# Performance work log

Measured on AMD Instinct MI355X. Metric: run time of the kernel, lower is better.

## Reference

```python
import jax, jax.numpy as jnp
import numpy as np

N_HID = 256
N_IN = 2
N_OUT = 2
BATCH = 256
LENGTH = 1024
ALPHA = 0.25
SIGMA_NEU = 0.05
N_CON = 6553


def setup_inputs() -> dict:
    key = jax.random.key(0)
    k1, k2, k3, k4, k5 = jax.random.split(key, 5)
    rng = np.random.RandomState(0)
    # masked recurrent weight pieces (match torch __init__ construction)
    w_0 = rng.randn(N_HID, N_HID) / np.sqrt(N_HID)
    abs_w_0 = jnp.asarray(np.abs(w_0), dtype=jnp.float32)
    is_con_np = np.zeros((N_HID, N_HID), dtype=np.float32)
    ind_in = rng.choice(np.arange(N_HID), size=N_CON)
    ind_out = rng.choice(np.arange(N_HID), size=N_CON)
    is_con_np[ind_in, ind_out] = 1.0
    w_sign = jnp.asarray(np.sign(rng.randn(N_HID, N_HID)), dtype=jnp.float32)
    is_con = jnp.asarray(is_con_np)
    return {
        "input_signal": jax.random.normal(k1, (BATCH, LENGTH, N_IN), dtype=jnp.float32),
        "hidden": jnp.zeros((BATCH, N_HID), dtype=jnp.float32),
        "w_in": jax.random.normal(k2, (N_HID, N_IN), dtype=jnp.float32) / np.sqrt(N_IN),
        "w_out": jax.random.normal(k3, (N_OUT, N_HID), dtype=jnp.float32) / np.sqrt(N_HID),
        "abs_w_0": abs_w_0,
        "w_sign": w_sign,
        "is_con": is_con,
    }


def reference(input_signal, hidden, w_in, w_out, abs_w_0, w_sign, is_con):
    # masked signed recurrent weight: theta = |w0| * mask; w_hh = sign * theta where mask>0
    theta = abs_w_0 * is_con
    w_hh = jnp.where(is_con > 0, w_sign * theta, jnp.zeros_like(theta))  # [H,H]

    alpha = jnp.full((N_HID,), ALPHA, dtype=input_signal.dtype)
    x = jnp.transpose(input_signal, (1, 0, 2))  # [T,B,I]
    # input projection for all timesteps at once (w_in has no bias)
    inp_proj = jnp.einsum("tbi,hi->tbh", x, w_in)  # [T,B,H]
    # iid per-step neural noise: randn * sigma * sqrt(alpha)
    noise = (jax.random.normal(jax.random.key(42), (LENGTH, BATCH, N_HID), dtype=input_signal.dtype)
             * SIGMA_NEU * jnp.sqrt(alpha))

    def step(h, uv):
        u, n = uv
        tmp = u + jnp.tanh(h) @ w_hh.T  # F.linear(tanh(h), w_hh)
        h_new = (1.0 - alpha) * h + alpha * tmp + n
        return h_new, h_new

    h_last, hs = jax.lax.scan(step, hidden, (inp_proj, noise))  # hs: [T,B,H]
    outputs = jnp.einsum("tbh,oh->tbo", hs, w_out)  # [T,B,O]
    hidden_list = jnp.transpose(hs, (1, 0, 2))  # [B,T,H]
    output_list = jnp.transpose(outputs, (1, 0, 2))  # [B,T,O]
    return hidden_list, output_list, h_last
```

## Files before the change

kernel.cpp:

```cpp
#include <hip/hip_runtime.h>
#include <stdint.h>

#define TT 1024
#define HB 256
#define NE 48
#define O1 67108864u
#define O2 (67108864u + 524288u)

__device__ __forceinline__ uint32_t rotl32(uint32_t x, uint32_t r){ return (x<<r)|(x>>(32u-r)); }

#define RND(r) { x0+=x1; x1=rotl32(x1,(r)); x1^=x0; }
__device__ __forceinline__ void tf_h1g(uint32_t k0,uint32_t k1,uint32_t ks2,uint32_t& x0,uint32_t& x1){
  x0 += k0; x1 += k1;
  RND(13) RND(15) RND(26) RND(6)  x0+=k1;  x1+=ks2+1u;
  RND(17) RND(29) RND(16) RND(24) x0+=ks2; x1+=k0+2u;
  RND(13) RND(15) RND(26) RND(6)  x0+=k0;  x1+=k1+3u;
}
__device__ __forceinline__ void tf_h2g(uint32_t k0,uint32_t k1,uint32_t ks2,uint32_t& x0,uint32_t& x1){
  RND(17) RND(29) RND(16) RND(24) x0+=k1;  x1+=ks2+4u;
  RND(13) RND(15) RND(26) RND(6)  x0+=ks2; x1+=k0+5u;
}
__device__ __forceinline__ void tf2x32(uint32_t k0,uint32_t k1,uint32_t& x0,uint32_t& x1){
  const uint32_t ks2 = 0x1BD11BDAu ^ k0 ^ k1;
  tf_h1g(k0,k1,ks2,x0,x1); tf_h2g(k0,k1,ks2,x0,x1);
}
__device__ __forceinline__ void tf_h1(uint32_t& x0, uint32_t& x1){ tf_h1g(0u,42u,0x1BD11BF0u,x0,x1); }
__device__ __forceinline__ void tf_h2(uint32_t& x0, uint32_t& x1){ tf_h2g(0u,42u,0x1BD11BF0u,x0,x1); }
#undef RND

__device__ __forceinline__ float bits_to_noise(uint32_t bits){
  float f = __uint_as_float((bits>>9) | 0x3F800000u) - 1.0f;
  const float lo = -0.99999994f;
  float x = fmaxf(fmaf(f, 1.99999994f, lo), lo);
  float m = (1.0f - x) * (1.0f + x);
  float w = -0.69314718056f * __log2f(m);
  float p;
  if (w < 5.0f){
    w -= 2.5f;
    p = 2.81022636e-08f;
    p = fmaf(p, w, 3.43273939e-07f);
    p = fmaf(p, w, -3.5233877e-06f);
    p = fmaf(p, w, -4.39150654e-06f);
    p = fmaf(p, w, 0.00021858087f);
    p = fmaf(p, w, -0.00125372503f);
    p = fmaf(p, w, -0.00417768164f);
    p = fmaf(p, w, 0.246640727f);
    p = fmaf(p, w, 1.50140941f);
  } else {
    w = __fsqrt_rn(w) - 3.0f;
    p = -0.000200214257f;
    p = fmaf(p, w, 0.000100950558f);
    p = fmaf(p, w, 0.00134934322f);
    p = fmaf(p, w, -0.00367342844f);
    p = fmaf(p, w, 0.00573950773f);
    p = fmaf(p, w, -0.0076224613f);
    p = fmaf(p, w, 0.00943887047f);
    p = fmaf(p, w, 1.00167406f);
    p = fmaf(p, w, 2.83297682f);
  }
  return 0.035355339059f * (p * x);
}

__global__ void init_flags(uint32_t* flags){
  if (flags) { flags[0]=0u; flags[1]=0u; }
}

__global__ void check_kernel(float* out, const uint32_t* flags){
  uint32_t a0=0u, a1=0u;                 tf2x32(0u,0u,a0,a1);
  uint32_t b0=0xffffffffu, b1=0xffffffffu; tf2x32(0xffffffffu,0xffffffffu,b0,b1);
  uint32_t c0=0x243f6a88u, c1=0x85a308d3u; tf2x32(0x13198a2eu,0x03707344u,c0,c1);
  if (!(a0==0x6b200159u && a1==0x99ba4efeu)) out[0] = 1e30f;
  if (!(b0==0x1cb996fcu && b1==0xbb002be7u)) out[1] = 2e30f;
  if (!(c0==0xc4923a9cu && c1==0x483df7a0u)) out[2] = 3e30f;
  uint32_t d0=7u, d1=9u; tf_h1(d0,d1); tf_h2(d0,d1);
  uint32_t e0=7u, e1=9u; tf2x32(0u,42u,e0,e1);
  if (!(d0==e0 && d1==e1)) out[3] = 4e30f;
  if (flags && flags[0]) out[5] = 6e30f;
}

__launch_bounds__(512)
__global__ void rnn_kernel(const float* __restrict__ input_signal,
                           const float* __restrict__ hidden0,
                           const float* __restrict__ w_in,
                           const float* __restrict__ w_out,
                           const float* __restrict__ abs_w0,
                           const float* __restrict__ w_sign,
                           const float* __restrict__ is_con,
                           float* __restrict__ out,
                           uint32_t* __restrict__ flags)
{
  __shared__ float    ew[HB][NE];
  __shared__ uint16_t ei[HB][NE];
  __shared__ float    xbuf[TT*2];
  __shared__ float    hstage[8][HB];
  __shared__ float    nbuf[4][HB];
  __shared__ float    tbuf[2][HB];
  __shared__ int      cnts[HB];
  __shared__ int      rankinv[HB];
  __shared__ int      rof4[HB];
  __shared__ float    wot0[HB], wot1[HB];

  const int tid = threadIdx.x;
  const int b   = blockIdx.x;
  const bool gw = (tid < HB);

  {
    const float* xg = input_signal + (uint64_t)b*TT*2;
    *(float4*)(xbuf + tid*4) = *(const float4*)(xg + tid*4);
  }
  if (gw){
    int c = 0;
    const float* ic = is_con + tid*HB;
    for (int k = 0; k < HB; k += 4){
      float4 c4 = *(const float4*)(ic + k);
      c += (c4.x>0.f)+(c4.y>0.f)+(c4.z>0.f)+(c4.w>0.f);
    }
    cnts[tid] = c;
    if (c > NE && flags) flags[0] = 1u;
  }
  __syncthreads();

  if (gw){
    int myc = cnts[tid], r = 0;
    for (int k = 0; k < HB; ++k){
      int ck = cnts[k];
      r += (int)((ck > myc) || (ck == myc && k < tid));
    }
    rankinv[r] = tid;
    rof4[tid]  = r << 2;
  }
  __syncthreads();

  uint32_t bj = 0u, ax0 = 0u, ax1 = 0u;
  if (gw){
    const int j = tid;
    const float* ic = is_con + j*HB;
    const float* aw = abs_w0 + j*HB;
    const float* ws = w_sign + j*HB;
    int n = 0;
    for (int k = 0; k < HB; ++k){
      if (ic[k] > 0.f && n < NE){
        ew[j][n] = ws[k]*aw[k];
        ei[j][n] = (uint16_t)rof4[k];
        ++n;
      }
    }
    for (int s = n; s < NE; ++s){ ew[j][s] = 0.f; ei[j][s] = (uint16_t)rof4[j]; }
    wot0[rof4[j]>>2] = w_out[j];
    wot1[rof4[j]>>2] = w_out[HB + j];
  } else {
    int m = tid - HB;
    int rowm = rankinv[m];
    bj = (uint32_t)b*256u + (uint32_t)rowm;
    uint32_t x0 = 0u, x1 = bj;
    tf2x32(0u, 42u, x0, x1);
    nbuf[0][m] = bits_to_noise(x0 ^ x1);
    ax0 = 0u; ax1 = 65536u + bj;
    tf_h1(ax0, ax1);
  }
  __syncthreads();

  float    pwv[NE];
  uint32_t piv[NE/2];
  int trip = 0, row = 0;
  float h = 0.f, wi0 = 0.f, wi1 = 0.f;
  float4 wo0 = {0,0,0,0}, wo1 = {0,0,0,0};
  if (gw){
    row = rankinv[tid];
    #pragma unroll
    for (int s = 0; s < NE; ++s) pwv[s] = ew[row][s];
    #pragma unroll
    for (int s = 0; s < NE/2; ++s) piv[s] = *(const uint32_t*)(&ei[row][2*s]);
    int c = cnts[row];
    trip = __builtin_amdgcn_readfirstlane((c + 3) & ~3);
    h   = hidden0[b*HB + row];
    wi0 = w_in[row*2]; wi1 = w_in[row*2 + 1];
    tbuf[0][tid] = 1.0f - 2.0f/(__expf(2.0f*h) + 1.0f);
  } else if (tid < HB + 64){
    int lam = tid - HB;
    wo0 = *(const float4*)(wot0 + lam*4);
    wo1 = *(const float4*)(wot1 + lam*4);
  }
  float* hrow = out + (uint64_t)b*TT*HB;
  float* orow = out + O1 + (uint64_t)b*TT*2;
  __syncthreads();

  for (int t = 0; t < TT; ++t){
    const int par = t & 1;
    if (gw){
      const char* tb = (const char*)(&tbuf[par][0]);
      float y0 = 0.f, y1 = 0.f;
      #pragma unroll
      for (int s = 0; s < NE; s += 4){
        if (s < trip){
          uint32_t pa = piv[s>>1], pb = piv[(s>>1)+1];
          float t0 = *(const float*)(tb + (pa & 0xFFFFu));
          float t1 = *(const float*)(tb + (pa >> 16));
          float t2 = *(const float*)(tb + (pb & 0xFFFFu));
          float t3 = *(const float*)(tb + (pb >> 16));
          y0 = fmaf(pwv[s+0], t0, y0);
          y1 = fmaf(pwv[s+1], t1, y1);
          y0 = fmaf(pwv[s+2], t2, y0);
          y1 = fmaf(pwv[s+3], t3, y1);
        }
      }
      float nz = nbuf[t&3][tid];
      float2 xv = *(const float2*)(xbuf + t*2);
      float u  = fmaf(xv.x, wi0, xv.y*wi1);
      h = fmaf(0.25f, u + y0 + y1, 0.75f*h) + nz;
      hstage[t&7][tid] = h;
      tbuf[par^1][tid] = 1.0f - 2.0f/(__expf(2.0f*h) + 1.0f);
    } else {
      int m = tid - HB;
      if (t < TT-1){
        uint32_t f0 = ax0, f1 = ax1;
        tf_h2(f0, f1);
        nbuf[(t+1)&3][m] = bits_to_noise(f0 ^ f1);
      }
      if (t < TT-2){
        ax0 = 0u; ax1 = (uint32_t)(t+2)*65536u + bj;
        tf_h1(ax0, ax1);
      }
      if (m < 64 && t > 0){
        float4 hv = *(const float4*)(&hstage[(t-1)&7][m*4]);
        float p0 = hv.x*wo0.x + hv.y*wo0.y + hv.z*wo0.z + hv.w*wo0.w;
        float p1 = hv.x*wo1.x + hv.y*wo1.y + hv.z*wo1.z + hv.w*wo1.w;
        #pragma unroll
        for (int d = 1; d < 64; d <<= 1){
          p0 += __shfl_xor(p0, d, 64);
          p1 += __shfl_xor(p1, d, 64);
        }
        if (m == 0) *(float2*)(orow + (t-1)*2) = make_float2(p0, p1);
      }
    }
    __syncthreads();

    if ((t & 7) == 7){
      int s  = tid >> 6;
      int j0 = (tid & 63) << 2;
      int4 rk = *(const int4*)(rof4 + j0);
      const char* hs = (const char*)(&hstage[s][0]);
      float4 v;
      v.x = *(const float*)(hs + rk.x);
      v.y = *(const float*)(hs + rk.y);
      v.z = *(const float*)(hs + rk.z);
      v.w = *(const float*)(hs + rk.w);
      *(float4*)(hrow + (uint64_t)(t - 7 + s)*HB + j0) = v;
      __syncthreads();
    }
  }

  if (!gw && (tid - HB) < 64){
    int m = tid - HB;
    float4 hv = *(const float4*)(&hstage[7][m*4]);
    float p0 = hv.x*wo0.x + hv.y*wo0.y + hv.z*wo0.z + hv.w*wo0.w;
    float p1 = hv.x*wo1.x + hv.y*wo1.y + hv.z*wo1.z + hv.w*wo1.w;
    #pragma unroll
    for (int d = 1; d < 64; d <<= 1){
      p0 += __shfl_xor(p0, d, 64);
      p1 += __shfl_xor(p1, d, 64);
    }
    if (m == 0) *(float2*)(orow + (TT-1)*2) = make_float2(p0, p1);
  }
  if (gw) out[O2 + b*HB + row] = h;
}

extern "C" void kernel_launch(void* const* d_in, const int* in_sizes, int n_in,
                              void* d_out, int out_size, void* d_ws, size_t ws_size,
                              hipStream_t stream) {
  const float* input_signal = (const float*)d_in[0];
  const float* hidden       = (const float*)d_in[1];
  const float* w_in         = (const float*)d_in[2];
  const float* w_out        = (const float*)d_in[3];
  const float* abs_w0       = (const float*)d_in[4];
  const float* w_sign       = (const float*)d_in[5];
  const float* is_con       = (const float*)d_in[6];
  float* out = (float*)d_out;
  uint32_t* flags = (ws_size >= 8) ? (uint32_t*)d_ws : nullptr;

  init_flags<<<1, 1, 0, stream>>>(flags);
  rnn_kernel<<<256, 512, 0, stream>>>(input_signal, hidden, w_in, w_out,
                                      abs_w0, w_sign, is_con, out, flags);
  check_kernel<<<1, 1, 0, stream>>>(out, flags);
}
```

Baseline: 1.023 ms.

## Split each hidden row across two lanes and double block size to 1024 threads

The block grows from 512 to 1024 threads. Each recurrent row is now computed by two lanes, each handling half of the sparse entries, and the halves are combined with a shuffle, which halves the serial per-step gather chain. The noise-generation and output-projection threads are also reorganised: 512 helper threads alternate between computing two timesteps of noise on even steps and projecting two delayed hidden states on odd steps. In exchange there are more waves per barrier, a shuffle on the critical path, idle odd lanes during the update, and the per-row register budget is halved under the larger launch bound.

```diff
diff --git a/kernel.cpp b/kernel.cpp
--- a/kernel.cpp
+++ b/kernel.cpp
@@ -4,28 +4,22 @@
 #define TT 1024
 #define HB 256
 #define NE 48
+#define NE2 24
 #define O1 67108864u
 #define O2 (67108864u + 524288u)
 
 __device__ __forceinline__ uint32_t rotl32(uint32_t x, uint32_t r){ return (x<<r)|(x>>(32u-r)); }
 
 #define RND(r) { x0+=x1; x1=rotl32(x1,(r)); x1^=x0; }
-__device__ __forceinline__ void tf_h1g(uint32_t k0,uint32_t k1,uint32_t ks2,uint32_t& x0,uint32_t& x1){
+__device__ __forceinline__ void tf2x32(uint32_t k0,uint32_t k1,uint32_t& x0,uint32_t& x1){
+  const uint32_t ks2 = 0x1BD11BDAu ^ k0 ^ k1;
   x0 += k0; x1 += k1;
   RND(13) RND(15) RND(26) RND(6)  x0+=k1;  x1+=ks2+1u;
   RND(17) RND(29) RND(16) RND(24) x0+=ks2; x1+=k0+2u;
   RND(13) RND(15) RND(26) RND(6)  x0+=k0;  x1+=k1+3u;
-}
-__device__ __forceinline__ void tf_h2g(uint32_t k0,uint32_t k1,uint32_t ks2,uint32_t& x0,uint32_t& x1){
   RND(17) RND(29) RND(16) RND(24) x0+=k1;  x1+=ks2+4u;
   RND(13) RND(15) RND(26) RND(6)  x0+=ks2; x1+=k0+5u;
 }
-__device__ __forceinline__ void tf2x32(uint32_t k0,uint32_t k1,uint32_t& x0,uint32_t& x1){
-  const uint32_t ks2 = 0x1BD11BDAu ^ k0 ^ k1;
-  tf_h1g(k0,k1,ks2,x0,x1); tf_h2g(k0,k1,ks2,x0,x1);
-}
-__device__ __forceinline__ void tf_h1(uint32_t& x0, uint32_t& x1){ tf_h1g(0u,42u,0x1BD11BF0u,x0,x1); }
-__device__ __forceinline__ void tf_h2(uint32_t& x0, uint32_t& x1){ tf_h2g(0u,42u,0x1BD11BF0u,x0,x1); }
 #undef RND
 
 __device__ __forceinline__ float bits_to_noise(uint32_t bits){
@@ -72,13 +66,10 @@
   if (!(a0==0x6b200159u && a1==0x99ba4efeu)) out[0] = 1e30f;
   if (!(b0==0x1cb996fcu && b1==0xbb002be7u)) out[1] = 2e30f;
   if (!(c0==0xc4923a9cu && c1==0x483df7a0u)) out[2] = 3e30f;
-  uint32_t d0=7u, d1=9u; tf_h1(d0,d1); tf_h2(d0,d1);
-  uint32_t e0=7u, e1=9u; tf2x32(0u,42u,e0,e1);
-  if (!(d0==e0 && d1==e1)) out[3] = 4e30f;
   if (flags && flags[0]) out[5] = 6e30f;
 }
 
-__launch_bounds__(512)
+__launch_bounds__(1024)
 __global__ void rnn_kernel(const float* __restrict__ input_signal,
                            const float* __restrict__ hidden0,
                            const float* __restrict__ w_in,
@@ -102,13 +93,13 @@
 
   const int tid = threadIdx.x;
   const int b   = blockIdx.x;
-  const bool gw = (tid < HB);
+  const bool gw = (tid < 512);
 
   {
     const float* xg = input_signal + (uint64_t)b*TT*2;
-    *(float4*)(xbuf + tid*4) = *(const float4*)(xg + tid*4);
-  }
-  if (gw){
+    *(float2*)(xbuf + tid*2) = *(const float2*)(xg + tid*2);
+  }
+  if (tid < HB){
     int c = 0;
     const float* ic = is_con + tid*HB;
     for (int k = 0; k < HB; k += 4){
@@ -120,7 +111,7 @@
   }
   __syncthreads();
 
-  if (gw){
+  if (tid < HB){
     int myc = cnts[tid], r = 0;
     for (int k = 0; k < HB; ++k){
       int ck = cnts[k];
@@ -131,8 +122,8 @@
   }
   __syncthreads();
 
-  uint32_t bj = 0u, ax0 = 0u, ax1 = 0u;
-  if (gw){
+  uint32_t bj = 0u;
+  if (tid < HB){
     const int j = tid;
     const float* ic = is_con + j*HB;
     const float* aw = abs_w0 + j*HB;
@@ -148,38 +139,54 @@
     for (int s = n; s < NE; ++s){ ew[j][s] = 0.f; ei[j][s] = (uint16_t)rof4[j]; }
     wot0[rof4[j]>>2] = w_out[j];
     wot1[rof4[j]>>2] = w_out[HB + j];
-  } else {
-    int m = tid - HB;
-    int rowm = rankinv[m];
-    bj = (uint32_t)b*256u + (uint32_t)rowm;
-    uint32_t x0 = 0u, x1 = bj;
-    tf2x32(0u, 42u, x0, x1);
-    nbuf[0][m] = bits_to_noise(x0 ^ x1);
-    ax0 = 0u; ax1 = 65536u + bj;
-    tf_h1(ax0, ax1);
-  }
-  __syncthreads();
-
-  float    pwv[NE];
-  uint32_t piv[NE/2];
-  int trip = 0, row = 0;
+  } else if (tid >= 512){
+    int m = tid - 512, rn = m >> 1, qn = m & 1;
+    bj = (uint32_t)b*256u + (uint32_t)rankinv[rn];
+    if (qn == 0){
+      uint32_t x0 = 0u, x1 = bj;
+      tf2x32(0u, 42u, x0, x1);
+      nbuf[0][rn] = bits_to_noise(x0 ^ x1);
+    }
+  }
+  __syncthreads();
+
+  float    pwv[NE2];
+  uint32_t piv[NE2/2];
+  int trip = 0, row = 0, q = 0, rr = 0;
   float h = 0.f, wi0 = 0.f, wi1 = 0.f;
   float4 wo0 = {0,0,0,0}, wo1 = {0,0,0,0};
+  int rf0 = 0, rf1 = 0;
+  {
+    int j0 = (tid & 127) << 1;
+    rf0 = rof4[j0]; rf1 = rof4[j0+1];
+  }
   if (gw){
-    row = rankinv[tid];
+    rr = tid >> 1; q = tid & 1;
+    row = rankinv[rr];
+    int c = cnts[row]; if (c > NE) c = NE;
+    uint16_t pad = (uint16_t)rof4[row];
+    uint32_t cur = 0u;
     #pragma unroll
-    for (int s = 0; s < NE; ++s) pwv[s] = ew[row][s];
-    #pragma unroll
-    for (int s = 0; s < NE/2; ++s) piv[s] = *(const uint32_t*)(&ei[row][2*s]);
-    int c = cnts[row];
-    trip = __builtin_amdgcn_readfirstlane((c + 3) & ~3);
-    h   = hidden0[b*HB + row];
-    wi0 = w_in[row*2]; wi1 = w_in[row*2 + 1];
-    tbuf[0][tid] = 1.0f - 2.0f/(__expf(2.0f*h) + 1.0f);
-  } else if (tid < HB + 64){
-    int lam = tid - HB;
-    wo0 = *(const float4*)(wot0 + lam*4);
-    wo1 = *(const float4*)(wot1 + lam*4);
+    for (int s = 0; s < NE2; ++s){
+      int idx = 2*s + q;
+      float w = 0.f; uint32_t o = pad;
+      if (idx < c){ w = ew[row][idx]; o = ei[row][idx]; }
+      pwv[s] = w;
+      if (s & 1) piv[s>>1] = cur | (o << 16); else cur = o;
+    }
+    trip = __builtin_amdgcn_readfirstlane((c + 1) >> 1);
+    if (q == 0){
+      h   = hidden0[b*HB + row];
+      wi0 = w_in[row*2]; wi1 = w_in[row*2 + 1];
+      tbuf[0][rr] = 1.0f - 2.0f/(__expf(2.0f*h) + 1.0f);
+    }
+  } else {
+    int m = tid - 512;
+    if (m < 128){
+      int lam = m & 63;
+      wo0 = *(const float4*)(wot0 + lam*4);
+      wo1 = *(const float4*)(wot1 + lam*4);
+    }
   }
   float* hrow = out + (uint64_t)b*TT*HB;
   float* orow = out + O1 + (uint64_t)b*TT*2;
@@ -191,78 +198,79 @@
       const char* tb = (const char*)(&tbuf[par][0]);
       float y0 = 0.f, y1 = 0.f;
       #pragma unroll
-      for (int s = 0; s < NE; s += 4){
+      for (int s = 0; s < NE2; s += 2){
         if (s < trip){
-          uint32_t pa = piv[s>>1], pb = piv[(s>>1)+1];
+          uint32_t pa = piv[s>>1];
           float t0 = *(const float*)(tb + (pa & 0xFFFFu));
           float t1 = *(const float*)(tb + (pa >> 16));
-          float t2 = *(const float*)(tb + (pb & 0xFFFFu));
-          float t3 = *(const float*)(tb + (pb >> 16));
-          y0 = fmaf(pwv[s+0], t0, y0);
+          y0 = fmaf(pwv[s],   t0, y0);
           y1 = fmaf(pwv[s+1], t1, y1);
-          y0 = fmaf(pwv[s+2], t2, y0);
-          y1 = fmaf(pwv[s+3], t3, y1);
         }
       }
-      float nz = nbuf[t&3][tid];
-      float2 xv = *(const float2*)(xbuf + t*2);
-      float u  = fmaf(xv.x, wi0, xv.y*wi1);
-      h = fmaf(0.25f, u + y0 + y1, 0.75f*h) + nz;
-      hstage[t&7][tid] = h;
-      tbuf[par^1][tid] = 1.0f - 2.0f/(__expf(2.0f*h) + 1.0f);
+      float y = y0 + y1;
+      y += __shfl_xor(y, 1, 64);
+      if (q == 0){
+        float nz = nbuf[t&3][rr];
+        float2 xv = *(const float2*)(xbuf + t*2);
+        float u  = fmaf(xv.x, wi0, xv.y*wi1);
+        h = fmaf(0.25f, u + y, 0.75f*h) + nz;
+        hstage[t&7][rr] = h;
+        tbuf[par^1][rr] = 1.0f - 2.0f/(__expf(2.0f*h) + 1.0f);
+      }
     } else {
-      int m = tid - HB;
-      if (t < TT-1){
-        uint32_t f0 = ax0, f1 = ax1;
-        tf_h2(f0, f1);
-        nbuf[(t+1)&3][m] = bits_to_noise(f0 ^ f1);
-      }
-      if (t < TT-2){
-        ax0 = 0u; ax1 = (uint32_t)(t+2)*65536u + bj;
-        tf_h1(ax0, ax1);
-      }
-      if (m < 64 && t > 0){
-        float4 hv = *(const float4*)(&hstage[(t-1)&7][m*4]);
-        float p0 = hv.x*wo0.x + hv.y*wo0.y + hv.z*wo0.z + hv.w*wo0.w;
-        float p1 = hv.x*wo1.x + hv.y*wo1.y + hv.z*wo1.z + hv.w*wo1.w;
-        #pragma unroll
-        for (int d = 1; d < 64; d <<= 1){
-          p0 += __shfl_xor(p0, d, 64);
-          p1 += __shfl_xor(p1, d, 64);
+      int m = tid - 512;
+      if (!(t & 1)){
+        int tv = t + 1 + (m & 1);
+        if (tv < TT){
+          uint32_t x0 = 0u, x1 = (uint32_t)tv*65536u + bj;
+          tf2x32(0u, 42u, x0, x1);
+          nbuf[tv&3][m>>1] = bits_to_noise(x0 ^ x1);
         }
-        if (m == 0) *(float2*)(orow + (t-1)*2) = make_float2(p0, p1);
+      } else if (m < 128){
+        int tau = t - 2 + (m >> 6);
+        if (tau >= 0){
+          int lam = m & 63;
+          float4 hv = *(const float4*)(&hstage[tau&7][lam*4]);
+          float p0 = hv.x*wo0.x + hv.y*wo0.y + hv.z*wo0.z + hv.w*wo0.w;
+          float p1 = hv.x*wo1.x + hv.y*wo1.y + hv.z*wo1.z + hv.w*wo1.w;
+          #pragma unroll
+          for (int d = 1; d < 64; d <<= 1){
+            p0 += __shfl_xor(p0, d, 64);
+            p1 += __shfl_xor(p1, d, 64);
+          }
+          if (lam == 0) *(float2*)(orow + tau*2) = make_float2(p0, p1);
+        }
       }
     }
     __syncthreads();
 
     if ((t & 7) == 7){
-      int s  = tid >> 6;
-      int j0 = (tid & 63) << 2;
-      int4 rk = *(const int4*)(rof4 + j0);
+      int s  = tid >> 7;
+      int j0 = (tid & 127) << 1;
       const char* hs = (const char*)(&hstage[s][0]);
-      float4 v;
-      v.x = *(const float*)(hs + rk.x);
-      v.y = *(const float*)(hs + rk.y);
-      v.z = *(const float*)(hs + rk.z);
-      v.w = *(const float*)(hs + rk.w);
-      *(float4*)(hrow + (uint64_t)(t - 7 + s)*HB + j0) = v;
+      float2 v;
+      v.x = *(const float*)(hs + rf0);
+      v.y = *(const float*)(hs + rf1);
+      *(float2*)(hrow + (uint64_t)(t - 7 + s)*HB + j0) = v;
       __syncthreads();
     }
   }
 
-  if (!gw && (tid - HB) < 64){
-    int m = tid - HB;
-    float4 hv = *(const float4*)(&hstage[7][m*4]);
-    float p0 = hv.x*wo0.x + hv.y*wo0.y + hv.z*wo0.z + hv.w*wo0.w;
-    float p1 = hv.x*wo1.x + hv.y*wo1.y + hv.z*wo1.z + hv.w*wo1.w;
-    #pragma unroll
-    for (int d = 1; d < 64; d <<= 1){
-      p0 += __shfl_xor(p0, d, 64);
-      p1 += __shfl_xor(p1, d, 64);
-    }
-    if (m == 0) *(float2*)(orow + (TT-1)*2) = make_float2(p0, p1);
-  }
-  if (gw) out[O2 + b*HB + row] = h;
+  if (!gw){
+    int m = tid - 512;
+    if (m < 64){
+      float4 hv = *(const float4*)(&hstage[7][m*4]);
+      float p0 = hv.x*wo0.x + hv.y*wo0.y + hv.z*wo0.z + hv.w*wo0.w;
+      float p1 = hv.x*wo1.x + hv.y*wo1.y + hv.z*wo1.z + hv.w*wo1.w;
+      #pragma unroll
+      for (int d = 1; d < 64; d <<= 1){
+        p0 += __shfl_xor(p0, d, 64);
+        p1 += __shfl_xor(p1, d, 64);
+      }
+      if (m == 0) *(float2*)(orow + (TT-1)*2) = make_float2(p0, p1);
+    }
+  }
+  if (gw && q == 0) out[O2 + b*HB + row] = h;
 }
 
 extern "C" void kernel_launch(void* const* d_in, const int* in_sizes, int n_in,
@@ -279,7 +287,7 @@
   uint32_t* flags = (ws_size >= 8) ? (uint32_t*)d_ws : nullptr;
 
   init_flags<<<1, 1, 0, stream>>>(flags);
-  rnn_kernel<<<256, 512, 0, stream>>>(input_signal, hidden, w_in, w_out,
-                                      abs_w0, w_sign, is_con, out, flags);
+  rnn_kernel<<<256, 1024, 0, stream>>>(input_signal, hidden, w_in, w_out,
+                                       abs_w0, w_sign, is_con, out, flags);
   check_kernel<<<1, 1, 0, stream>>>(out, flags);
 }
```

Result: faster. 893.4 us (-12.6%).
